# Kernel tuning notes

Hardware: AMD Instinct MI355X
Metric: run time of the kernel (lower is better)

## Reference

```python
import jax, jax.numpy as jnp
import numpy as np

K_MAX_X = 16
K_MAX_T = 16


def _k_actual(N, k_max):
    # low-mode indices [0..k_max] ++ [N-k_max..N-1], mapped to signed frequencies
    idx = np.concatenate([np.arange(k_max + 1), np.arange(N - k_max, N)]).astype(np.float32)
    return np.where(idx <= (N - 1) // 2, idx, idx - N)


def _phase(N, k_max, sign):
    # separable 1D truncated DFT factor: exp(sign*2*pi*i*k*n/N)/sqrt(N), shape [modes, N]
    k = _k_actual(N, k_max)
    n = np.arange(N, dtype=np.float32)
    ang = sign * 2.0 * np.pi * k[:, None] * n[None, :] / N
    return jnp.asarray((np.exp(1j * ang) / np.sqrt(N)).astype(np.complex64))


def setup_inputs() -> dict:
    key = jax.random.key(0)
    k1, k2, k3 = jax.random.split(key, 3)
    B, C_in, C_out, H, W = 16, 64, 64, 128, 128
    modes = 2 * K_MAX_X + 1  # 33
    scale = 1.0 / (C_in * C_out)
    x = jax.random.normal(k1, (B, C_in, H, W), dtype=jnp.float32)
    wr = scale * jax.random.uniform(k2, (C_in, C_out, modes, modes), dtype=jnp.float32)
    wi = scale * jax.random.uniform(k3, (C_in, C_out, modes, modes), dtype=jnp.float32)
    return {"x": x, "weights_real": wr, "weights_imag": wi}


def reference(x, weights_real, weights_imag):
    B, C, H, W = x.shape
    Px_f = _phase(H, K_MAX_X, -1.0)  # [mx, H]
    Pt_f = _phase(W, K_MAX_T, -1.0)  # [mt, W]
    Px_i = _phase(H, K_MAX_X, +1.0)
    Pt_i = _phase(W, K_MAX_T, +1.0)
    xc = x.astype(jnp.complex64)
    # truncated 2D DFT (separable): X[b,c,i,j]
    X = jnp.einsum('bcnm,in,jm->bcij', xc, Px_f, Pt_f)
    R = (weights_real + 1j * weights_imag).astype(jnp.complex64)
    out_kept = jnp.einsum('bcij,coij->boij', X, R)
    # truncated inverse DFT back to grid
    out = jnp.einsum('boij,in,jm->bonm', out_kept, Px_i, Pt_i)
    return jnp.real(out)
```

## Files before the change

kernel.cpp:

```cpp
#include <hip/hip_runtime.h>


#define NB   16
#define NC   64
#define NO   64
#define NH   128
#define NW   128
#define NM   33
#define WMODE (NM*NM)
#define MPAD  1104
#define NIMG 1024

typedef __attribute__((ext_vector_type(8))) short s8v;
typedef __attribute__((ext_vector_type(4))) float f4v;

__device__ inline unsigned short f2bf(float f) {
  union { float f; unsigned u; } v; v.f = f;
  unsigned r = (v.u + 0x7FFFu + ((v.u >> 16) & 1u)) >> 16;
  return (unsigned short)r;
}

__device__ inline s8v pack8(float4 a, float4 b) {
  s8v r;
  r[0] = (short)f2bf(a.x); r[1] = (short)f2bf(a.y);
  r[2] = (short)f2bf(a.z); r[3] = (short)f2bf(a.w);
  r[4] = (short)f2bf(b.x); r[5] = (short)f2bf(b.y);
  r[6] = (short)f2bf(b.z); r[7] = (short)f2bf(b.w);
  return r;
}

__device__ inline uint2 pack4(f4v a) {
  uint2 p;
  p.x = (unsigned)f2bf(a[0]) | ((unsigned)f2bf(a[1]) << 16);
  p.y = (unsigned)f2bf(a[2]) | ((unsigned)f2bf(a[3]) << 16);
  return p;
}

__device__ inline unsigned short phase_bf(int f, int x) {
  if (f >= 66) return 0;
  int g = (f < 33) ? f : f - 33;
  int fr = (g <= 16) ? g : g + 95;
  int ph = (fr * x) & 127;
  float ang = (float)ph * 0.04908738521234052f;
  float v = ((f < 33) ? cosf(ang) : sinf(ang)) * 0.08838834764831845f;
  return f2bf(v);
}

__global__ __launch_bounds__(256) void spc_tables(short* __restrict__ T1,
                                                  short* __restrict__ T2,
                                                  short* __restrict__ T3,
                                                  short* __restrict__ T4) {
  int tid = blockIdx.x * 256 + threadIdx.x;
  if (tid >= 49152) return;
  int f, x; short* dst;
  if (tid < 10240) {
    int e = tid & 7, l = (tid >> 3) & 63, q = tid >> 9;
    int ks = q / 5, jt = q - 5 * ks;
    f = jt * 16 + (l & 15); x = ks * 32 + (l >> 4) * 8 + e; dst = T1 + tid;
  } else if (tid < 20480) {
    int u = tid - 10240;
    int e = u & 7, l = (u >> 3) & 63, q = u >> 9;
    int it = q >> 2, ks = q & 3;
    f = it * 16 + (l & 15); x = ks * 32 + (l >> 4) * 8 + e; dst = T2 + u;
  } else if (tid < 36864) {
    int u = tid - 20480;
    int e = u & 7, l = (u >> 3) & 63, q = u >> 9;
    int cs = q >> 4, ks = (q >> 3) & 1, mt = q & 7;
    int j = ks * 32 + (l >> 4) * 8 + e;
    f = (j < 33) ? cs * 33 + j : 66;
    x = mt * 16 + (l & 15); dst = T3 + u;
  } else {
    int u = tid - 36864;
    int e = u & 7, l = (u >> 3) & 63, q = u >> 9;
    int nt = q / 3, ks = q - 3 * nt;
    int i2 = ks * 32 + (l >> 4) * 8 + e;
    if (i2 < 48) f = (i2 < 33) ? i2 : 66;
    else         f = (i2 - 48 < 33) ? 33 + (i2 - 48) : 66;
    x = nt * 16 + (l & 15); dst = T4 + u;
  }
  *dst = (short)phase_bf(f, x);
}

__global__ __launch_bounds__(256) void spc_wrepack(const float* __restrict__ wr,
                                                   const float* __restrict__ wi,
                                                   short* __restrict__ Wfrag) {
  __shared__ unsigned short Ls[64 * 16 * 17];
  const int t = threadIdx.x;
  const int ot = blockIdx.x;
  const int mg = blockIdx.y;
  const int m0 = mg * 16;
  const int oo = t >> 4, mm = t & 15;
  int msrc = m0 + mm; if (msrc > 1088) msrc = 1088;

  for (int pl = 0; pl < 2; ++pl) {
    const float* src = pl ? wi : wr;
    __syncthreads();
    for (int c = 0; c < 64; ++c) {
      float v = src[(size_t)(c * 64 + ot * 16 + oo) * WMODE + msrc];
      Ls[(c * 16 + oo) * 17 + mm] = f2bf(v);
    }
    __syncthreads();
    for (int pass = 0; pass < 8; ++pass) {
      int p = pass * 4 + (t >> 6);
      int m_l = p >> 1, ks = p & 1;
      int l = t & 63;
      int lr = l & 15, lg = l >> 4;
      unsigned short v[8];
#pragma unroll
      for (int e = 0; e < 8; ++e)
        v[e] = Ls[((ks * 32 + lg * 8 + e) * 16 + lr) * 17 + m_l];
      uint4 u;
      u.x = (unsigned)v[0] | ((unsigned)v[1] << 16);
      u.y = (unsigned)v[2] | ((unsigned)v[3] << 16);
      u.z = (unsigned)v[4] | ((unsigned)v[5] << 16);
      u.w = (unsigned)v[6] | ((unsigned)v[7] << 16);
      size_t frag = (((size_t)(m0 + m_l) * 4 + ot) * 2 + pl) * 2 + ks;
      *reinterpret_cast<uint4*>(Wfrag + frag * 512 + l * 8) = u;
    }
  }
}

__global__ __launch_bounds__(256) void spc_fwd_mfma(const float* __restrict__ x,
                                                    const s8v* __restrict__ T1,
                                                    const s8v* __restrict__ T2,
                                                    unsigned* __restrict__ X2u) {
  __shared__ short Wt[80 * 128];
  __shared__ float Gs[80 * 84];
  const int t = threadIdx.x;
  const int l = t & 63;
  const int w = t >> 6;
  const int lr = l & 15;
  const int lg = l >> 4;
  const int img = blockIdx.x;
  const float* xp = x + (size_t)img * (NH * NW);

  for (int nn = 0; nn < 2; ++nn) {
    const int nt = 2 * w + nn;
    const float* xrow = xp + (nt * 16 + lr) * NW + lg * 8;
    s8v a[4];
#pragma unroll
    for (int ks = 0; ks < 4; ++ks) {
      float4 f0 = *reinterpret_cast<const float4*>(xrow + ks * 32);
      float4 f1 = *reinterpret_cast<const float4*>(xrow + ks * 32 + 4);
      a[ks] = pack8(f0, f1);
    }
#pragma unroll
    for (int jt = 0; jt < 5; ++jt) {
      f4v acc = {0.f, 0.f, 0.f, 0.f};
#pragma unroll
      for (int ks = 0; ks < 4; ++ks) {
        s8v b = T1[(ks * 5 + jt) * 64 + l];
        acc = __builtin_amdgcn_mfma_f32_16x16x32_bf16(a[ks], b, acc, 0, 0, 0);
      }
      int j = jt * 16 + lr;
      int g = ((nt * 16 + lg * 4) >> 2) ^ ((j & 7) << 2);
      *reinterpret_cast<uint2*>(&Wt[j * 128 + g * 4]) = pack4(acc);
    }
  }
  __syncthreads();

  for (int tix = w; tix < 25; tix += 4) {
    int it = tix / 5, j2 = tix - 5 * it;
    int jrow = j2 * 16 + lr;
    f4v acc = {0.f, 0.f, 0.f, 0.f};
#pragma unroll
    for (int ks = 0; ks < 4; ++ks) {
      s8v afr = T2[(it * 4 + ks) * 64 + l];
      int g = (ks * 8 + lg * 2) ^ ((jrow & 7) << 2);
      s8v b = *reinterpret_cast<const s8v*>(&Wt[jrow * 128 + g * 4]);
      acc = __builtin_amdgcn_mfma_f32_16x16x32_bf16(afr, b, acc, 0, 0, 0);
    }
    int gi = it * 16 + lg * 4;
#pragma unroll
    for (int r = 0; r < 4; ++r) Gs[(gi + r) * 84 + jrow] = acc[r];
  }
  __syncthreads();

  unsigned* X2p = X2u + (size_t)img * WMODE;
  for (int idx = t; idx < WMODE; idx += 256) {
    int i = idx / 33, j = idx - 33 * i;
    float g11 = Gs[i * 84 + j];
    float g22 = Gs[(i + 33) * 84 + (j + 33)];
    float g12 = Gs[i * 84 + (j + 33)];
    float g21 = Gs[(i + 33) * 84 + j];
    X2p[idx] = (unsigned)f2bf(g11 - g22) | ((unsigned)f2bf(-(g12 + g21)) << 16);
  }
}

__global__ __launch_bounds__(256) void spc_xrepack(const unsigned* __restrict__ X2u,
                                                   unsigned* __restrict__ Xp) {
  __shared__ unsigned Ls[64 * 65];
  const int t = threadIdx.x;
  const int l = t & 63;
  const int w = t >> 6;
  const int m0 = blockIdx.x * 64;
  const int c0 = blockIdx.y * 4;

  for (int rr = 0; rr < 16; ++rr) {
    int r = w * 16 + rr;
    int b = r & 15, cl = r >> 4;
    int m = m0 + l;
    unsigned v = 0;
    if (m < WMODE) v = X2u[(size_t)(b * 64 + c0 + cl) * WMODE + m];
    Ls[r * 65 + l] = v;
  }
  __syncthreads();
  for (int p = 0; p < 16; ++p) {
    int m_l = p * 4 + w;
    int m = m0 + m_l;
    if (m >= WMODE) continue;
    int cl = l >> 4, b = l & 15;
    unsigned v = Ls[(cl * 16 + b) * 65 + m_l];
    Xp[((size_t)m * 64 + c0 + cl) * 16 + b] = v;
  }
}

__global__ __launch_bounds__(256) void spc_mix_mfma(const unsigned* __restrict__ Xp,
                                                    const s8v* __restrict__ Wfrag,
                                                    short* __restrict__ Kbf) {
  __shared__ short Kls[4 * 2 * 64 * 16];
  const int t = threadIdx.x;
  const int l = t & 63;
  const int w = t >> 6;
  const int lr = l & 15;
  const int lg = l >> 4;
  const int mg = blockIdx.x;
  int m = mg * 4 + w; if (m > 1088) m = 1088;

  s8v xr[2], xi[2], nxi[2];
#pragma unroll
  for (int ks = 0; ks < 2; ++ks) {
#pragma unroll
    for (int e = 0; e < 8; ++e) {
      unsigned u = Xp[((size_t)m * 64 + ks * 32 + lg * 8 + e) * 16 + lr];
      xr[ks][e] = (short)(u & 0xFFFFu);
      unsigned short hi = (unsigned short)(u >> 16);
      xi[ks][e] = (short)hi;
      nxi[ks][e] = (short)(hi ^ 0x8000u);
    }
  }

  const s8v* Wm = Wfrag + (size_t)m * 16 * 64;
#pragma unroll
  for (int ot = 0; ot < 4; ++ot) {
    s8v rr0 = Wm[((ot * 2 + 0) * 2 + 0) * 64 + l];
    s8v rr1 = Wm[((ot * 2 + 0) * 2 + 1) * 64 + l];
    s8v ri0 = Wm[((ot * 2 + 1) * 2 + 0) * 64 + l];
    s8v ri1 = Wm[((ot * 2 + 1) * 2 + 1) * 64 + l];
    f4v kr = {0.f, 0.f, 0.f, 0.f}, ki = {0.f, 0.f, 0.f, 0.f};
    kr = __builtin_amdgcn_mfma_f32_16x16x32_bf16(xr[0], rr0, kr, 0, 0, 0);
    kr = __builtin_amdgcn_mfma_f32_16x16x32_bf16(xr[1], rr1, kr, 0, 0, 0);
    kr = __builtin_amdgcn_mfma_f32_16x16x32_bf16(nxi[0], ri0, kr, 0, 0, 0);
    kr = __builtin_amdgcn_mfma_f32_16x16x32_bf16(nxi[1], ri1, kr, 0, 0, 0);
    ki = __builtin_amdgcn_mfma_f32_16x16x32_bf16(xr[0], ri0, ki, 0, 0, 0);
    ki = __builtin_amdgcn_mfma_f32_16x16x32_bf16(xr[1], ri1, ki, 0, 0, 0);
    ki = __builtin_amdgcn_mfma_f32_16x16x32_bf16(xi[0], rr0, ki, 0, 0, 0);
    ki = __builtin_amdgcn_mfma_f32_16x16x32_bf16(xi[1], rr1, ki, 0, 0, 0);
    *reinterpret_cast<uint2*>(&Kls[((w * 2 + 0) * 64 + ot * 16 + lr) * 16 + lg * 4]) = pack4(kr);
    *reinterpret_cast<uint2*>(&Kls[((w * 2 + 1) * 64 + ot * 16 + lr) * 16 + lg * 4]) = pack4(ki);
  }
  __syncthreads();

#pragma unroll
  for (int rep = 0; rep < 4; ++rep) {
    int img = rep * 256 + t;
    int b = img >> 6, o = img & 63;
#pragma unroll
    for (int ri = 0; ri < 2; ++ri) {
      unsigned short v[4];
#pragma unroll
      for (int mm = 0; mm < 4; ++mm)
        v[mm] = (unsigned short)Kls[((mm * 2 + ri) * 64 + o) * 16 + b];
      uint2 u;
      u.x = (unsigned)v[0] | ((unsigned)v[1] << 16);
      u.y = (unsigned)v[2] | ((unsigned)v[3] << 16);
      *reinterpret_cast<uint2*>(Kbf + ((size_t)(mg * 1024 + img) * 2 + ri) * 4) = u;
    }
  }
}

__global__ __launch_bounds__(256) void spc_inv_mfma(const short* __restrict__ Kbf,
                                                    const s8v* __restrict__ T3,
                                                    const s8v* __restrict__ T4,
                                                    float* __restrict__ out) {
  __shared__ short Kls2[2 * MPAD];
  __shared__ short Vt[128 * 128];
  const int t = threadIdx.x;
  const int l = t & 63;
  const int w = t >> 6;
  const int lr = l & 15;
  const int lg = l >> 4;
  const int img = blockIdx.x;

  {
    const uint2* src = reinterpret_cast<const uint2*>(Kbf);
    uint2* dstl = reinterpret_cast<uint2*>(Kls2);
    for (int g = t; g < 546; g += 256) {
      int mgi = g >> 1, ri = g & 1;
      dstl[ri * 276 + mgi] = src[((size_t)(mgi * 1024 + img)) * 2 + ri];
    }
  }
  __syncthreads();

  s8v fr[2][3][2];
#pragma unroll
  for (int ri2 = 0; ri2 < 2; ++ri2)
#pragma unroll
    for (int it = 0; it < 3; ++it)
#pragma unroll
      for (int ks = 0; ks < 2; ++ks) {
        const int i = it * 16 + lr;
#pragma unroll
        for (int e = 0; e < 8; ++e) {
          const int j = ks * 32 + lg * 8 + e;
          unsigned short v = (i < 33 && j < 33)
              ? (unsigned short)Kls2[ri2 * MPAD + i * 33 + j] : (unsigned short)0;
          fr[ri2][it][ks][e] = (short)v;
        }
      }

  for (int mm = 0; mm < 2; ++mm) {
    const int mt = w * 2 + mm;
    const int m = mt * 16 + lr;
    s8v cw[2], sw[2], nsw[2];
#pragma unroll
    for (int ks = 0; ks < 2; ++ks) {
      cw[ks] = T3[((0 * 2 + ks) * 8 + mt) * 64 + l];
      sw[ks] = T3[((1 * 2 + ks) * 8 + mt) * 64 + l];
#pragma unroll
      for (int e = 0; e < 8; ++e)
        nsw[ks][e] = (short)(((unsigned short)sw[ks][e]) ^ 0x8000u);
    }
#pragma unroll
    for (int it = 0; it < 3; ++it) {
      f4v t1 = {0.f, 0.f, 0.f, 0.f}, t2 = {0.f, 0.f, 0.f, 0.f};
#pragma unroll
      for (int ks = 0; ks < 2; ++ks) {
        t1 = __builtin_amdgcn_mfma_f32_16x16x32_bf16(fr[0][it][ks], cw[ks],  t1, 0, 0, 0);
        t1 = __builtin_amdgcn_mfma_f32_16x16x32_bf16(fr[1][it][ks], nsw[ks], t1, 0, 0, 0);
        t2 = __builtin_amdgcn_mfma_f32_16x16x32_bf16(fr[1][it][ks], cw[ks],  t2, 0, 0, 0);
        t2 = __builtin_amdgcn_mfma_f32_16x16x32_bf16(fr[0][it][ks], sw[ks],  t2, 0, 0, 0);
      }
      const int base1 = it * 16 + lg * 4;
      const int g1 = (base1 >> 2) ^ ((m & 7) << 2);
      *reinterpret_cast<uint2*>(&Vt[m * 128 + g1 * 4]) = pack4(t1);
      f4v nt2v = {-t2[0], -t2[1], -t2[2], -t2[3]};
      const int g2 = ((48 + base1) >> 2) ^ ((m & 7) << 2);
      *reinterpret_cast<uint2*>(&Vt[m * 128 + g2 * 4]) = pack4(nt2v);
    }
  }
  __syncthreads();

  float* op = out + (size_t)img * (NH * NW);
  for (int nn = 0; nn < 2; ++nn) {
    const int nt = w * 2 + nn;
    s8v a[3];
#pragma unroll
    for (int ks = 0; ks < 3; ++ks) a[ks] = T4[(nt * 3 + ks) * 64 + l];
    for (int mt = 0; mt < 8; ++mt) {
      const int m = mt * 16 + lr;
      f4v acc = {0.f, 0.f, 0.f, 0.f};
#pragma unroll
      for (int ks = 0; ks < 3; ++ks) {
        const int g = (ks * 8 + lg * 2) ^ ((m & 7) << 2);
        s8v bb = *reinterpret_cast<const s8v*>(&Vt[m * 128 + g * 4]);
        acc = __builtin_amdgcn_mfma_f32_16x16x32_bf16(a[ks], bb, acc, 0, 0, 0);
      }
      const int n = nt * 16 + lg * 4;
#pragma unroll
      for (int r = 0; r < 4; ++r) op[(n + r) * NW + m] = acc[r];
    }
  }
}

extern "C" void kernel_launch(void* const* d_in, const int* in_sizes, int n_in,
                              void* d_out, int out_size, void* d_ws, size_t ws_size,
                              hipStream_t stream) {
  const float* x  = (const float*)d_in[0];
  const float* wr = (const float*)d_in[1];
  const float* wi = (const float*)d_in[2];
  float* out = (float*)d_out;

  char* ws = (char*)d_ws;
  short* T1 = (short*)(ws);
  short* T2 = (short*)(ws + 20480);
  short* T3 = (short*)(ws + 40960);
  short* T4 = (short*)(ws + 73728);
  short* Wfrag = (short*)(ws + 98304);
  unsigned* X2u = (unsigned*)(ws + 18186240);
  short* Kbf = (short*)(ws + 18186240);
  unsigned* Xp = (unsigned*)(ws + 22659072);

  hipLaunchKernelGGL(spc_tables, dim3(192), dim3(256), 0, stream, T1, T2, T3, T4);
  hipLaunchKernelGGL(spc_wrepack, dim3(4, 69), dim3(256), 0, stream, wr, wi, Wfrag);
  hipLaunchKernelGGL(spc_fwd_mfma, dim3(NIMG), dim3(256), 0, stream,
                     x, (const s8v*)T1, (const s8v*)T2, X2u);
  hipLaunchKernelGGL(spc_xrepack, dim3(18, 16), dim3(256), 0, stream, X2u, Xp);
  hipLaunchKernelGGL(spc_mix_mfma, dim3(273), dim3(256), 0, stream,
                     Xp, (const s8v*)Wfrag, Kbf);
  hipLaunchKernelGGL(spc_inv_mfma, dim3(NIMG), dim3(256), 0, stream,
                     Kbf, (const s8v*)T3, (const s8v*)T4, out);
}
```

Measured before the change: 81.20 us.

## Split repack and mix kernels across more blocks and make Kbf image-contiguous

The weight repack, X repack and mode-mixing kernels now each use twice as many blocks (split over input-channel halves, channel pairs and output-channel halves), so a 256-CU part gets more parallelism. The mixing kernel now writes its spectral output in a per-image contiguous layout padded to MPAD=1092. The inverse kernel can then load each image's coefficients with a few coalesced 16-byte loads instead of strided 8-byte gathers. In exchange the mix kernel reloads its X fragments in both output-half blocks and scatters its writes across images.

```diff
diff --git a/kernel.cpp b/kernel.cpp
--- a/kernel.cpp
+++ b/kernel.cpp
@@ -8,7 +8,7 @@
 #define NW   128
 #define NM   33
 #define WMODE (NM*NM)
-#define MPAD  1104
+#define MPAD  1092
 #define NIMG 1024
 
 typedef __attribute__((ext_vector_type(8))) short s8v;
@@ -84,10 +84,11 @@
 __global__ __launch_bounds__(256) void spc_wrepack(const float* __restrict__ wr,
                                                    const float* __restrict__ wi,
                                                    short* __restrict__ Wfrag) {
-  __shared__ unsigned short Ls[64 * 16 * 17];
+  __shared__ unsigned short Ls[32 * 16 * 17];
   const int t = threadIdx.x;
   const int ot = blockIdx.x;
   const int mg = blockIdx.y;
+  const int cs = blockIdx.z;
   const int m0 = mg * 16;
   const int oo = t >> 4, mm = t & 15;
   int msrc = m0 + mm; if (msrc > 1088) msrc = 1088;
@@ -95,26 +96,25 @@
   for (int pl = 0; pl < 2; ++pl) {
     const float* src = pl ? wi : wr;
     __syncthreads();
-    for (int c = 0; c < 64; ++c) {
-      float v = src[(size_t)(c * 64 + ot * 16 + oo) * WMODE + msrc];
-      Ls[(c * 16 + oo) * 17 + mm] = f2bf(v);
+    for (int cl = 0; cl < 32; ++cl) {
+      float v = src[(size_t)((cs * 32 + cl) * 64 + ot * 16 + oo) * WMODE + msrc];
+      Ls[(cl * 16 + oo) * 17 + mm] = f2bf(v);
     }
     __syncthreads();
-    for (int pass = 0; pass < 8; ++pass) {
-      int p = pass * 4 + (t >> 6);
-      int m_l = p >> 1, ks = p & 1;
+    for (int pass = 0; pass < 4; ++pass) {
+      int m_l = pass * 4 + (t >> 6);
       int l = t & 63;
       int lr = l & 15, lg = l >> 4;
       unsigned short v[8];
 #pragma unroll
       for (int e = 0; e < 8; ++e)
-        v[e] = Ls[((ks * 32 + lg * 8 + e) * 16 + lr) * 17 + m_l];
+        v[e] = Ls[((lg * 8 + e) * 16 + lr) * 17 + m_l];
       uint4 u;
       u.x = (unsigned)v[0] | ((unsigned)v[1] << 16);
       u.y = (unsigned)v[2] | ((unsigned)v[3] << 16);
       u.z = (unsigned)v[4] | ((unsigned)v[5] << 16);
       u.w = (unsigned)v[6] | ((unsigned)v[7] << 16);
-      size_t frag = (((size_t)(m0 + m_l) * 4 + ot) * 2 + pl) * 2 + ks;
+      size_t frag = (((size_t)(m0 + m_l) * 4 + ot) * 2 + pl) * 2 + cs;
       *reinterpret_cast<uint4*>(Wfrag + frag * 512 + l * 8) = u;
     }
   }
@@ -189,15 +189,15 @@
 
 __global__ __launch_bounds__(256) void spc_xrepack(const unsigned* __restrict__ X2u,
                                                    unsigned* __restrict__ Xp) {
-  __shared__ unsigned Ls[64 * 65];
+  __shared__ unsigned Ls[32 * 65];
   const int t = threadIdx.x;
   const int l = t & 63;
   const int w = t >> 6;
   const int m0 = blockIdx.x * 64;
-  const int c0 = blockIdx.y * 4;
-
-  for (int rr = 0; rr < 16; ++rr) {
-    int r = w * 16 + rr;
+  const int c0 = blockIdx.y * 2;
+
+  for (int rr = 0; rr < 8; ++rr) {
+    int r = w * 8 + rr;
     int b = r & 15, cl = r >> 4;
     int m = m0 + l;
     unsigned v = 0;
@@ -205,11 +205,11 @@
     Ls[r * 65 + l] = v;
   }
   __syncthreads();
-  for (int p = 0; p < 16; ++p) {
-    int m_l = p * 4 + w;
+  for (int p = 0; p < 8; ++p) {
+    int m_l = p * 8 + w * 2 + (l >> 5);
     int m = m0 + m_l;
     if (m >= WMODE) continue;
-    int cl = l >> 4, b = l & 15;
+    int cl = (l >> 4) & 1, b = l & 15;
     unsigned v = Ls[(cl * 16 + b) * 65 + m_l];
     Xp[((size_t)m * 64 + c0 + cl) * 16 + b] = v;
   }
@@ -218,13 +218,14 @@
 __global__ __launch_bounds__(256) void spc_mix_mfma(const unsigned* __restrict__ Xp,
                                                     const s8v* __restrict__ Wfrag,
                                                     short* __restrict__ Kbf) {
-  __shared__ short Kls[4 * 2 * 64 * 16];
+  __shared__ short Kls[4 * 2 * 32 * 16];
   const int t = threadIdx.x;
   const int l = t & 63;
   const int w = t >> 6;
   const int lr = l & 15;
   const int lg = l >> 4;
   const int mg = blockIdx.x;
+  const int oh = blockIdx.y;
   int m = mg * 4 + w; if (m > 1088) m = 1088;
 
   s8v xr[2], xi[2], nxi[2];
@@ -242,7 +243,8 @@
 
   const s8v* Wm = Wfrag + (size_t)m * 16 * 64;
 #pragma unroll
-  for (int ot = 0; ot < 4; ++ot) {
+  for (int otl = 0; otl < 2; ++otl) {
+    const int ot = oh * 2 + otl;
     s8v rr0 = Wm[((ot * 2 + 0) * 2 + 0) * 64 + l];
     s8v rr1 = Wm[((ot * 2 + 0) * 2 + 1) * 64 + l];
     s8v ri0 = Wm[((ot * 2 + 1) * 2 + 0) * 64 + l];
@@ -256,25 +258,26 @@
     ki = __builtin_amdgcn_mfma_f32_16x16x32_bf16(xr[1], ri1, ki, 0, 0, 0);
     ki = __builtin_amdgcn_mfma_f32_16x16x32_bf16(xi[0], rr0, ki, 0, 0, 0);
     ki = __builtin_amdgcn_mfma_f32_16x16x32_bf16(xi[1], rr1, ki, 0, 0, 0);
-    *reinterpret_cast<uint2*>(&Kls[((w * 2 + 0) * 64 + ot * 16 + lr) * 16 + lg * 4]) = pack4(kr);
-    *reinterpret_cast<uint2*>(&Kls[((w * 2 + 1) * 64 + ot * 16 + lr) * 16 + lg * 4]) = pack4(ki);
-  }
-  __syncthreads();
-
-#pragma unroll
-  for (int rep = 0; rep < 4; ++rep) {
-    int img = rep * 256 + t;
-    int b = img >> 6, o = img & 63;
+    *reinterpret_cast<uint2*>(&Kls[((w * 2 + 0) * 32 + otl * 16 + lr) * 16 + lg * 4]) = pack4(kr);
+    *reinterpret_cast<uint2*>(&Kls[((w * 2 + 1) * 32 + otl * 16 + lr) * 16 + lg * 4]) = pack4(ki);
+  }
+  __syncthreads();
+
+#pragma unroll
+  for (int rep = 0; rep < 2; ++rep) {
+    int idx = rep * 256 + t;
+    int b = idx >> 5, ol = idx & 31;
+    size_t img = (size_t)b * 64 + oh * 32 + ol;
 #pragma unroll
     for (int ri = 0; ri < 2; ++ri) {
       unsigned short v[4];
 #pragma unroll
       for (int mm = 0; mm < 4; ++mm)
-        v[mm] = (unsigned short)Kls[((mm * 2 + ri) * 64 + o) * 16 + b];
+        v[mm] = (unsigned short)Kls[((mm * 2 + ri) * 32 + ol) * 16 + b];
       uint2 u;
       u.x = (unsigned)v[0] | ((unsigned)v[1] << 16);
       u.y = (unsigned)v[2] | ((unsigned)v[3] << 16);
-      *reinterpret_cast<uint2*>(Kbf + ((size_t)(mg * 1024 + img) * 2 + ri) * 4) = u;
+      *reinterpret_cast<uint2*>(Kbf + img * (2 * MPAD) + ri * MPAD + mg * 4) = u;
     }
   }
 }
@@ -293,12 +296,9 @@
   const int img = blockIdx.x;
 
   {
-    const uint2* src = reinterpret_cast<const uint2*>(Kbf);
-    uint2* dstl = reinterpret_cast<uint2*>(Kls2);
-    for (int g = t; g < 546; g += 256) {
-      int mgi = g >> 1, ri = g & 1;
-      dstl[ri * 276 + mgi] = src[((size_t)(mgi * 1024 + img)) * 2 + ri];
-    }
+    const uint4* src = reinterpret_cast<const uint4*>(Kbf + (size_t)img * (2 * MPAD));
+    uint4* dstl = reinterpret_cast<uint4*>(Kls2);
+    for (int idx = t; idx < 273; idx += 256) dstl[idx] = src[idx];
   }
   __syncthreads();
 
@@ -392,11 +392,11 @@
   unsigned* Xp = (unsigned*)(ws + 22659072);
 
   hipLaunchKernelGGL(spc_tables, dim3(192), dim3(256), 0, stream, T1, T2, T3, T4);
-  hipLaunchKernelGGL(spc_wrepack, dim3(4, 69), dim3(256), 0, stream, wr, wi, Wfrag);
+  hipLaunchKernelGGL(spc_wrepack, dim3(4, 69, 2), dim3(256), 0, stream, wr, wi, Wfrag);
   hipLaunchKernelGGL(spc_fwd_mfma, dim3(NIMG), dim3(256), 0, stream,
                      x, (const s8v*)T1, (const s8v*)T2, X2u);
-  hipLaunchKernelGGL(spc_xrepack, dim3(18, 16), dim3(256), 0, stream, X2u, Xp);
-  hipLaunchKernelGGL(spc_mix_mfma, dim3(273), dim3(256), 0, stream,
+  hipLaunchKernelGGL(spc_xrepack, dim3(18, 32), dim3(256), 0, stream, X2u, Xp);
+  hipLaunchKernelGGL(spc_mix_mfma, dim3(273, 2), dim3(256), 0, stream,
                      Xp, (const s8v*)Wfrag, Kbf);
   hipLaunchKernelGGL(spc_inv_mfma, dim3(NIMG), dim3(256), 0, stream,
                      Kbf, (const s8v*)T3, (const s8v*)T4, out);
```

After: 86.98 us. 7.1% more time.
